# Performance work log

Measured on AMD Instinct MI355X. Metric: run time of the kernel, lower is better.

## Reference

```python
import jax, jax.numpy as jnp
import numpy as np
import math

B, S, D, H = 4, 2048, 1024, 16
HD = D // H  # head_size = 64


def setup_inputs() -> dict:
    key = jax.random.key(0)
    ks = jax.random.split(key, 12)
    s = 1.0 / math.sqrt(D)
    inp = {
        "query_in": jax.random.normal(ks[0], (B, S, D), jnp.float32),
        "key_in": jax.random.normal(ks[1], (B, S, D), jnp.float32),
        "values_in": jax.random.normal(ks[2], (B, S, D), jnp.float32),
        # causal mask, broadcast over batch and heads
        "mask": jnp.tril(jnp.ones((S, S), jnp.int32))[None, None],
        "Wq": jax.random.normal(ks[3], (D, D), jnp.float32) * s,
        "bq": jnp.zeros((D,), jnp.float32),
        "Wk": jax.random.normal(ks[4], (D, D), jnp.float32) * s,
        "bk": jnp.zeros((D,), jnp.float32),
        "Wv": jax.random.normal(ks[5], (D, D), jnp.float32) * s,
        "bv": jnp.zeros((D,), jnp.float32),
        "Wo": jax.random.normal(ks[6], (D, D), jnp.float32) * s,
        "bo": jnp.zeros((D,), jnp.float32),
    }
    return inp


def _heads(x):
    # [B,S,D] -> [B,H,S,HD]
    return x.reshape(B, S, H, HD).transpose(0, 2, 1, 3)


def reference(query_in, key_in, values_in, mask, Wq, bq, Wk, bk, Wv, bv, Wo, bo):
    q = _heads(query_in @ Wq.T + bq)
    k = _heads(key_in @ Wk.T + bk)
    v = _heads(values_in @ Wv.T + bv)
    # scaled dot-product scores [B,H,Sq,Sk]
    att = jnp.einsum("bhqd,bhkd->bhqk", q, k) / math.sqrt(HD)
    att = jnp.where(mask == 0, jnp.float32(-1e9), att)
    # NOTE: original module applies dropout (identity at eval / p=0) directly
    # to scores with NO softmax -- faithfully reproduced here.
    out = jnp.einsum("bhqk,bhkd->bhqd", att, v)
    out = out.transpose(0, 2, 1, 3).reshape(B, S, D)
    return out @ Wo.T + bo
```

## Files before the change

### kernel.cpp

```cpp
#include <hip/hip_runtime.h>
#include <stdint.h>

typedef unsigned short ushort_t;
typedef __bf16 bf16x8 __attribute__((ext_vector_type(8)));
typedef float f32x4 __attribute__((ext_vector_type(4)));
typedef ushort_t us4 __attribute__((ext_vector_type(4)));

#define MFMA16(a, b, c) __builtin_amdgcn_mfma_f32_16x16x32_bf16((a), (b), (c), 0, 0, 0)

constexpr int Bn = 4, Sn = 2048, Dn = 1024, Hn = 16, HDn = 64;
constexpr float SCALE = 0.125f;
constexpr float NEG = -1e9f;

__device__ __forceinline__ float bf2f(ushort_t u) {
  unsigned x = ((unsigned)u) << 16;
  return __builtin_bit_cast(float, x);
}
__device__ __forceinline__ ushort_t f2bf(float f) {
  unsigned x = __builtin_bit_cast(unsigned, f);
  x = x + 0x7FFFu + ((x >> 16) & 1u);
  return (ushort_t)(x >> 16);
}
__device__ __forceinline__ uint4 ld8_f32_bf16(const float* __restrict__ p) {
  float4 a = *(const float4*)p;
  float4 b = *(const float4*)(p + 4);
  union { ushort_t u[8]; uint4 v; } r;
  r.u[0] = f2bf(a.x); r.u[1] = f2bf(a.y); r.u[2] = f2bf(a.z); r.u[3] = f2bf(a.w);
  r.u[4] = f2bf(b.x); r.u[5] = f2bf(b.y); r.u[6] = f2bf(b.z); r.u[7] = f2bf(b.w);
  return r.v;
}
__device__ __forceinline__ void gl2lds16(const void* g, void* l) {
  __builtin_amdgcn_global_load_lds(
      (__attribute__((address_space(1))) void*)g,
      (__attribute__((address_space(3))) void*)l, 16, 0, 0);
}

__global__ __launch_bounds__(256)
void cvt_all(const float* __restrict__ xq, const float* __restrict__ xk,
             const float* __restrict__ xv, const float* __restrict__ wq,
             const float* __restrict__ wk, const float* __restrict__ wv,
             const float* __restrict__ wo, ushort_t* __restrict__ Xd,
             ushort_t* __restrict__ Wd) {
  const int bid = blockIdx.x;
  if (bid < 12288) {
    const int which = bid >> 12;
    const float* s = which == 0 ? xq : which == 1 ? xk : xv;
    size_t i = ((size_t)(bid & 4095) * 256 + threadIdx.x) * 8;
    *(uint4*)(Xd + (size_t)which * 8388608 + i) = ld8_f32_bf16(s + i);
  } else {
    const int wb = bid - 12288, which = wb >> 9;
    const float* s = which == 0 ? wq : which == 1 ? wk : which == 2 ? wv : wo;
    size_t i = ((size_t)(wb & 511) * 256 + threadIdx.x) * 8;
    *(uint4*)(Wd + (size_t)which * 1048576 + i) = ld8_f32_bf16(s + i);
  }
}

__global__ __launch_bounds__(256, 4)
void gemm_qkv(const ushort_t* __restrict__ Xb, const ushort_t* __restrict__ Wb,
              const float* __restrict__ bq, const float* __restrict__ bk,
              const float* __restrict__ bv, ushort_t* __restrict__ Qd,
              ushort_t* __restrict__ Ktd, ushort_t* __restrict__ Vtd) {
  constexpr int K = 1024;
  __shared__ __align__(16) ushort_t As[128 * 64];
  __shared__ __align__(16) ushort_t Bs[128 * 64];

  const int z = blockIdx.z;
  const ushort_t* A  = Xb + (size_t)z * 8388608;
  const ushort_t* Wt = Wb + (size_t)z * 1048576;
  const float* bias = z == 0 ? bq : z == 1 ? bk : bv;
  ushort_t* Cp = z == 0 ? Qd : z == 1 ? Ktd : Vtd;

  const int tid = threadIdx.x;
  const int lane = tid & 63, w = tid >> 6;
  const int quad = lane >> 4, l16 = lane & 15;
  const int wm = w >> 1, wn = w & 1;
  const int row0 = blockIdx.x * 128;
  const int col0 = blockIdx.y * 128;

  const int sr = lane >> 3;
  const int sg = ((lane & 7) ^ (sr & 7)) * 8;
  const ushort_t* Ab = A  + (size_t)(row0 + w * 32 + sr) * K + sg;
  const ushort_t* Bb = Wt + (size_t)(col0 + w * 32 + sr) * K + sg;

  f32x4 acc[4][4] = {};

  for (int k0 = 0; k0 < K; k0 += 64) {
    __syncthreads();
#pragma unroll
    for (int i = 0; i < 4; ++i) {
      gl2lds16(Ab + (size_t)(i * 8) * K + k0, &As[(w * 32 + i * 8) * 64]);
      gl2lds16(Bb + (size_t)(i * 8) * K + k0, &Bs[(w * 32 + i * 8) * 64]);
    }
    __syncthreads();
#pragma unroll
    for (int ks = 0; ks < 2; ++ks) {
      const int kg = ((ks * 4 + quad) ^ (l16 & 7)) * 8;
      bf16x8 af[4], bfr[4];
#pragma unroll
      for (int mt = 0; mt < 4; ++mt)
        af[mt] = *(const bf16x8*)(&As[(wm * 64 + mt * 16 + l16) * 64 + kg]);
#pragma unroll
      for (int nt = 0; nt < 4; ++nt)
        bfr[nt] = *(const bf16x8*)(&Bs[(wn * 64 + nt * 16 + l16) * 64 + kg]);
#pragma unroll
      for (int mt = 0; mt < 4; ++mt)
#pragma unroll
        for (int nt = 0; nt < 4; ++nt)
          acc[mt][nt] = MFMA16(af[mt], bfr[nt], acc[mt][nt]);
    }
  }

#pragma unroll
  for (int mt = 0; mt < 4; ++mt) {
#pragma unroll
    for (int nt = 0; nt < 4; ++nt) {
      const int col = col0 + wn * 64 + nt * 16 + l16;
      const float bv4 = bias[col];
      const int rowb = row0 + wm * 64 + mt * 16 + quad * 4;
      if (z != 0) {
        const int b = rowb >> 11, s = rowb & (Sn - 1);
        const int h = col >> 6, hd = col & 63;
        us4 pk;
#pragma unroll
        for (int r = 0; r < 4; ++r) pk[r] = f2bf(acc[mt][nt][r] + bv4);
        *(us4*)(Cp + ((size_t)((b * Hn + h) * HDn + hd)) * Sn + s) = pk;
      } else {
#pragma unroll
        for (int r = 0; r < 4; ++r) {
          const int row = rowb + r;
          const int b = row >> 11, s = row & (Sn - 1);
          const int h = col >> 6, hd = col & 63;
          Cp[(((size_t)(b * Hn + h) * Sn + s) << 6) + hd] = f2bf(acc[mt][nt][r] + bv4);
        }
      }
    }
  }
}

__global__ __launch_bounds__(256, 4)
void gemm_out(const ushort_t* __restrict__ A, const ushort_t* __restrict__ Wt,
              const float* __restrict__ bias, float* __restrict__ Cp) {
  constexpr int K = 1024;
  __shared__ __align__(16) ushort_t As[128 * 64];
  __shared__ __align__(16) ushort_t Bs[128 * 64];

  const int tid = threadIdx.x;
  const int lane = tid & 63, w = tid >> 6;
  const int quad = lane >> 4, l16 = lane & 15;
  const int wm = w >> 1, wn = w & 1;
  const int row0 = blockIdx.x * 128;
  const int col0 = blockIdx.y * 128;

  const int sr = lane >> 3;
  const int sg = ((lane & 7) ^ (sr & 7)) * 8;
  const ushort_t* Ab = A  + (size_t)(row0 + w * 32 + sr) * K + sg;
  const ushort_t* Bb = Wt + (size_t)(col0 + w * 32 + sr) * K + sg;

  f32x4 acc[4][4] = {};

  for (int k0 = 0; k0 < K; k0 += 64) {
    __syncthreads();
#pragma unroll
    for (int i = 0; i < 4; ++i) {
      gl2lds16(Ab + (size_t)(i * 8) * K + k0, &As[(w * 32 + i * 8) * 64]);
      gl2lds16(Bb + (size_t)(i * 8) * K + k0, &Bs[(w * 32 + i * 8) * 64]);
    }
    __syncthreads();
#pragma unroll
    for (int ks = 0; ks < 2; ++ks) {
      const int kg = ((ks * 4 + quad) ^ (l16 & 7)) * 8;
      bf16x8 af[4], bfr[4];
#pragma unroll
      for (int mt = 0; mt < 4; ++mt)
        af[mt] = *(const bf16x8*)(&As[(wm * 64 + mt * 16 + l16) * 64 + kg]);
#pragma unroll
      for (int nt = 0; nt < 4; ++nt)
        bfr[nt] = *(const bf16x8*)(&Bs[(wn * 64 + nt * 16 + l16) * 64 + kg]);
#pragma unroll
      for (int mt = 0; mt < 4; ++mt)
#pragma unroll
        for (int nt = 0; nt < 4; ++nt)
          acc[mt][nt] = MFMA16(af[mt], bfr[nt], acc[mt][nt]);
    }
  }

#pragma unroll
  for (int mt = 0; mt < 4; ++mt)
#pragma unroll
    for (int nt = 0; nt < 4; ++nt) {
      const int col = col0 + wn * 64 + nt * 16 + l16;
      const float bv = bias[col];
      const int rowb = row0 + wm * 64 + mt * 16 + quad * 4;
#pragma unroll
      for (int r = 0; r < 4; ++r)
        Cp[(size_t)(rowb + r) * 1024 + col] = acc[mt][nt][r] + bv;
    }
}

__global__ __launch_bounds__(256)
void gtile(const ushort_t* __restrict__ Kt, const ushort_t* __restrict__ Vt,
           float* __restrict__ Gd, float* __restrict__ Rs) {
  __shared__ __align__(16) ushort_t Kts[4096];
  __shared__ __align__(16) ushort_t Vts[4096];
  __shared__ float tsum[64];
  const int tid = threadIdx.x, lane = tid & 63, w = tid >> 6;
  const int quad = lane >> 4, l16 = lane & 15;
  const int t = blockIdx.x, bh = blockIdx.y;
  const ushort_t* Ktb = Kt + (size_t)bh * HDn * Sn;
  const ushort_t* Vtb = Vt + (size_t)bh * HDn * Sn;

  const int sr = lane >> 3;
  const int sg = ((lane & 7) ^ (sr & 7)) * 8;

  if (tid < 64) tsum[tid] = 0.f;
#pragma unroll
  for (int c = 0; c < 2; ++c) {
    const int row = w * 16 + c * 8;
    gl2lds16(Ktb + (size_t)(row + sr) * Sn + t * 64 + sg, &Kts[row * 64]);
    gl2lds16(Vtb + (size_t)(row + sr) * Sn + t * 64 + sg, &Vts[row * 64]);
  }
  __syncthreads();

  f32x4 zacc[4] = {};
#pragma unroll
  for (int ks = 0; ks < 2; ++ks) {
    const int kg = ((ks * 4 + quad) ^ (l16 & 7)) * 8;
    bf16x8 ak = *(const bf16x8*)(&Kts[(w * 16 + l16) * 64 + kg]);
#pragma unroll
    for (int nt = 0; nt < 4; ++nt) {
      bf16x8 bv8 = *(const bf16x8*)(&Vts[(nt * 16 + l16) * 64 + kg]);
      zacc[nt] = MFMA16(ak, bv8, zacc[nt]);
    }
  }
  float* gd = Gd + (size_t)(bh * 32 + t) * 4096;
#pragma unroll
  for (int nt = 0; nt < 4; ++nt)
    *(f32x4*)(gd + (nt * 16 + l16) * 64 + w * 16 + quad * 4) = zacc[nt];

  {
    const int n = tid & 63, j = tid >> 6;
    float p = 0.f;
#pragma unroll
    for (int gg2 = 0; gg2 < 2; ++gg2) {
      const int g = 2 * j + gg2;
      union { uint4 v; ushort_t u[8]; } c;
      c.v = *(const uint4*)(&Vts[n * 64 + ((g ^ (n & 7)) << 3)]);
#pragma unroll
      for (int e = 0; e < 8; ++e) p += bf2f(c.u[e]);
    }
    atomicAdd(&tsum[n], p);
  }
  __syncthreads();
  if (tid < 64) Rs[(size_t)(bh * 32 + t) * 64 + tid] = tsum[tid];
}

__global__ __launch_bounds__(256)
void scan_attn(const ushort_t* __restrict__ Q, const ushort_t* __restrict__ Kt,
               const ushort_t* __restrict__ Vt, const float* __restrict__ Gd,
               const float* __restrict__ Rs, ushort_t* __restrict__ O) {
  __shared__ __align__(16) ushort_t Vts[2][4096];
  __shared__ __align__(16) ushort_t Zs[4096];
  __shared__ __align__(16) ushort_t Ks[4096];
  __shared__ __align__(16) ushort_t Ss[64][72];
  __shared__ __align__(16) float sfx[4][64];

  const int tid = threadIdx.x, lane = tid & 63, w = tid >> 6;
  const int quad = lane >> 4, l16 = lane & 15;
  const int bh = blockIdx.x;
  const int g = blockIdx.y;
  const int qt0 = g * 4;
  const int b = bh >> 4, h = bh & 15;
  const ushort_t* Qb  = Q  + (size_t)bh * Sn * HDn;
  const ushort_t* Ktb = Kt + (size_t)bh * HDn * Sn;
  const ushort_t* Vtb = Vt + (size_t)bh * HDn * Sn;
  const float* Gb = Gd + (size_t)bh * 32 * 4096;
  const float* Rb = Rs + (size_t)bh * 32 * 64;

  const int sr = lane >> 3;
  const int sg = ((lane & 7) ^ (sr & 7)) * 8;
  const int q8 = lane & 7, h8 = lane >> 3;

  const int zn = tid >> 2, zd0 = (tid & 3) * 16;
  const float* gthr = Gb + zn * 64 + zd0;

  uint4  kvr[2][2];
  bf16x8 bqr[2][2];
  f32x4  gq[2][4];

  {
    const int q0 = qt0 * 64;
#pragma unroll
    for (int c = 0; c < 2; ++c) {
      const int row = w * 16 + c * 8;
      gl2lds16(Vtb + (size_t)(row + sr) * Sn + q0 + sg, &Vts[0][row * 64]);
      kvr[0][c] = *(const uint4*)(Ktb + (size_t)(w * 16 + c * 8 + h8) * Sn + q0 + q8 * 8);
    }
#pragma unroll
    for (int ks = 0; ks < 2; ++ks)
      bqr[0][ks] = *(const bf16x8*)(Qb + (size_t)(q0 + w * 16 + l16) * HDn + (ks * 4 + quad) * 8);
#pragma unroll
    for (int j = 0; j < 4; ++j)
      gq[0][j] = *(const f32x4*)(gthr + (size_t)qt0 * 4096 + 4 * j);
  }

  if (tid < 64) {
    float acc = 0.f;
    for (int tau = 31; tau >= qt0; --tau) {
      if (tau < qt0 + 4) sfx[tau - qt0][tid] = acc;
      acc += Rb[(size_t)tau * 64 + tid];
    }
  }

  f32x4 Zacc[4] = {};
#pragma unroll 4
  for (int tau = 0; tau < qt0; ++tau) {
#pragma unroll
    for (int j = 0; j < 4; ++j)
      Zacc[j] += *(const f32x4*)(gthr + (size_t)tau * 4096 + 4 * j);
  }

#pragma unroll 4
  for (int i = 0; i < 4; ++i) {
    const int cur = i & 1;
    const int qt = qt0 + i, q0 = qt * 64;

    __syncthreads();

#pragma unroll
    for (int j = 0; j < 4; ++j) {
      const int d = zd0 + 4 * j;
      us4 pk;
#pragma unroll
      for (int r = 0; r < 4; ++r) pk[r] = f2bf(SCALE * Zacc[j][r]);
      *(us4*)(&Zs[zn * 64 + (((d >> 3) ^ (zn & 7)) << 3) + (d & 7)]) = pk;
    }
#pragma unroll
    for (int c = 0; c < 2; ++c) {
      const int hd = w * 16 + c * 8 + h8;
      const int G = hd >> 3;
      const ushort_t* ku = (const ushort_t*)&kvr[cur][c];
#pragma unroll
      for (int j = 0; j < 8; ++j) {
        const int e = (j + q8) & 7;
        const int s = q8 * 8 + e;
        Ks[s * 64 + ((G ^ e) << 3) + (hd & 7)] = ku[e];
      }
    }

    __syncthreads();

    if (i < 3) {
      const int q1 = (qt + 1) * 64, nxt = 1 - cur;
#pragma unroll
      for (int c = 0; c < 2; ++c) {
        const int row = w * 16 + c * 8;
        gl2lds16(Vtb + (size_t)(row + sr) * Sn + q1 + sg, &Vts[nxt][row * 64]);
        kvr[nxt][c] = *(const uint4*)(Ktb + (size_t)(w * 16 + c * 8 + h8) * Sn + q1 + q8 * 8);
      }
#pragma unroll
      for (int ks = 0; ks < 2; ++ks)
        bqr[nxt][ks] = *(const bf16x8*)(Qb + (size_t)(q1 + w * 16 + l16) * HDn + (ks * 4 + quad) * 8);
#pragma unroll
      for (int j = 0; j < 4; ++j)
        gq[nxt][j] = *(const f32x4*)(gthr + (size_t)(qt + 1) * 4096 + 4 * j);
    }

    f32x4 oacc[4] = {};
#pragma unroll
    for (int ks = 0; ks < 2; ++ks) {
      const int kg = ((ks * 4 + quad) ^ (l16 & 7)) * 8;
#pragma unroll
      for (int nt = 0; nt < 4; ++nt) {
        bf16x8 az = *(const bf16x8*)(&Zs[(nt * 16 + l16) * 64 + kg]);
        oacc[nt] = MFMA16(az, bqr[cur][ks], oacc[nt]);
      }
    }
    f32x4 sacc[4] = {};
#pragma unroll
    for (int ks = 0; ks < 2; ++ks) {
      const int kg = ((ks * 4 + quad) ^ (l16 & 7)) * 8;
#pragma unroll
      for (int nt = 0; nt < 4; ++nt) {
        bf16x8 ak = *(const bf16x8*)(&Ks[(nt * 16 + l16) * 64 + kg]);
        sacc[nt] = MFMA16(ak, bqr[cur][ks], sacc[nt]);
      }
    }
    const int qrel = w * 16 + l16;
#pragma unroll
    for (int nt = 0; nt < 4; ++nt) {
      const int kb = nt * 16 + quad * 4;
      us4 pk;
#pragma unroll
      for (int r = 0; r < 4; ++r) {
        float val = (kb + r > qrel) ? NEG : sacc[nt][r] * SCALE;
        pk[r] = f2bf(val);
      }
      *(us4*)(&Ss[qrel][kb]) = pk;
    }
#pragma unroll
    for (int ks = 0; ks < 2; ++ks) {
      bf16x8 bs = *(const bf16x8*)(&Ss[qrel][ks * 32 + quad * 8]);
#pragma unroll
      for (int nt = 0; nt < 4; ++nt) {
        bf16x8 av = *(const bf16x8*)(&Vts[cur][(nt * 16 + l16) * 64 + (((ks * 4 + quad) ^ (l16 & 7)) << 3)]);
        oacc[nt] = MFMA16(av, bs, oacc[nt]);
      }
    }

    const int s = q0 + w * 16 + l16;
#pragma unroll
    for (int nt = 0; nt < 4; ++nt) {
      const int nb = nt * 16 + quad * 4;
      float4 s4 = *(const float4*)(&sfx[i][nb]);
      us4 pk;
      pk[0] = f2bf(oacc[nt][0] + NEG * s4.x);
      pk[1] = f2bf(oacc[nt][1] + NEG * s4.y);
      pk[2] = f2bf(oacc[nt][2] + NEG * s4.z);
      pk[3] = f2bf(oacc[nt][3] + NEG * s4.w);
      *(us4*)(&O[((size_t)(b * Sn + s)) * Dn + h * 64 + nb]) = pk;
    }

#pragma unroll
    for (int j = 0; j < 4; ++j) Zacc[j] += gq[cur][j];
  }
}

extern "C" void kernel_launch(void* const* d_in, const int* in_sizes, int n_in,
                              void* d_out, int out_size, void* d_ws, size_t ws_size,
                              hipStream_t stream) {
  const float* Xq = (const float*)d_in[0];
  const float* Xk = (const float*)d_in[1];
  const float* Xv = (const float*)d_in[2];
  const float* Wq = (const float*)d_in[4];
  const float* bq = (const float*)d_in[5];
  const float* Wk = (const float*)d_in[6];
  const float* bk = (const float*)d_in[7];
  const float* Wv = (const float*)d_in[8];
  const float* bv = (const float*)d_in[9];
  const float* Wo = (const float*)d_in[10];
  const float* bo = (const float*)d_in[11];

  constexpr size_t MiB = 1024 * 1024;
  char* ws = (char*)d_ws;
  ushort_t* Xb  = (ushort_t*)(ws);
  ushort_t* Wb  = (ushort_t*)(ws + 48 * MiB);
  ushort_t* Qb  = (ushort_t*)(ws + 56 * MiB);
  ushort_t* Ktb = (ushort_t*)(ws + 72 * MiB);
  ushort_t* Vtb = (ushort_t*)(ws + 88 * MiB);
  ushort_t* Ob  = (ushort_t*)(ws + 120 * MiB);
  float*    Gd  = (float*)   (ws + 144 * MiB);
  float*    Rsum= (float*)   (ws + 176 * MiB);

  cvt_all<<<14336, 256, 0, stream>>>(Xq, Xk, Xv, Wq, Wk, Wv, Wo, Xb, Wb);
  gemm_qkv<<<dim3(64, 8, 3), 256, 0, stream>>>(Xb, Wb, bq, bk, bv, Qb, Ktb, Vtb);
  gtile<<<dim3(32, 64), 256, 0, stream>>>(Ktb, Vtb, Gd, Rsum);
  scan_attn<<<dim3(64, 8), 256, 0, stream>>>(Qb, Ktb, Vtb, Gd, Rsum, Ob);
  gemm_out<<<dim3(64, 8), 256, 0, stream>>>(Ob, Wb + (size_t)3 * 1048576, bo,
                                            (float*)d_out);
}
```

Measured before the change: 303.5 us.

## Fuse K^T V prefix into scan kernel and V row sums into QKV GEMM

Removes the separate gtile kernel. V tile row sums are now computed in the QKV GEMM epilogue with shuffle reductions, and each scan_attn2 block computes its own K^T V prefix with MFMA over the preceding tiles using double-buffered LDS loads. This drops the fp32 Gd intermediate write and read and one kernel launch. In exchange it repeats prefix work across blocks, so later sequence groups get up to 28 tiles of extra MFMA, giving load imbalance. Row sums are also now taken from fp32 accumulators instead of bf16-rounded V.

New measurement: 290.7 us. -4.2%, faster.

```diff
diff --git a/kernel.cpp b/kernel.cpp
--- a/kernel.cpp
+++ b/kernel.cpp
@@ -59,7 +59,8 @@
 void gemm_qkv(const ushort_t* __restrict__ Xb, const ushort_t* __restrict__ Wb,
               const float* __restrict__ bq, const float* __restrict__ bk,
               const float* __restrict__ bv, ushort_t* __restrict__ Qd,
-              ushort_t* __restrict__ Ktd, ushort_t* __restrict__ Vtd) {
+              ushort_t* __restrict__ Ktd, ushort_t* __restrict__ Vtd,
+              float* __restrict__ Rs) {
   constexpr int K = 1024;
   __shared__ __align__(16) ushort_t As[128 * 64];
   __shared__ __align__(16) ushort_t Bs[128 * 64];
@@ -135,6 +136,27 @@
       }
     }
   }
+
+  if (z == 2) {
+    const int b = row0 >> 11;
+    const int t = ((row0 & (Sn - 1)) >> 6) + wm;
+#pragma unroll
+    for (int nt = 0; nt < 4; ++nt) {
+      const int col = col0 + wn * 64 + nt * 16 + l16;
+      const float bv4 = bias[col];
+      float p = 0.f;
+#pragma unroll
+      for (int mt = 0; mt < 4; ++mt)
+#pragma unroll
+        for (int r = 0; r < 4; ++r) p += acc[mt][nt][r] + bv4;
+      p += __shfl_xor(p, 16);
+      p += __shfl_xor(p, 32);
+      if (quad == 0) {
+        const int h = col >> 6, n = col & 63;
+        Rs[((size_t)(b * Hn + h) * 32 + t) * 64 + n] = p;
+      }
+    }
+  }
 }
 
 __global__ __launch_bounds__(256, 4)
@@ -198,66 +220,10 @@
 }
 
 __global__ __launch_bounds__(256)
-void gtile(const ushort_t* __restrict__ Kt, const ushort_t* __restrict__ Vt,
-           float* __restrict__ Gd, float* __restrict__ Rs) {
-  __shared__ __align__(16) ushort_t Kts[4096];
-  __shared__ __align__(16) ushort_t Vts[4096];
-  __shared__ float tsum[64];
-  const int tid = threadIdx.x, lane = tid & 63, w = tid >> 6;
-  const int quad = lane >> 4, l16 = lane & 15;
-  const int t = blockIdx.x, bh = blockIdx.y;
-  const ushort_t* Ktb = Kt + (size_t)bh * HDn * Sn;
-  const ushort_t* Vtb = Vt + (size_t)bh * HDn * Sn;
-
-  const int sr = lane >> 3;
-  const int sg = ((lane & 7) ^ (sr & 7)) * 8;
-
-  if (tid < 64) tsum[tid] = 0.f;
-#pragma unroll
-  for (int c = 0; c < 2; ++c) {
-    const int row = w * 16 + c * 8;
-    gl2lds16(Ktb + (size_t)(row + sr) * Sn + t * 64 + sg, &Kts[row * 64]);
-    gl2lds16(Vtb + (size_t)(row + sr) * Sn + t * 64 + sg, &Vts[row * 64]);
-  }
-  __syncthreads();
-
-  f32x4 zacc[4] = {};
-#pragma unroll
-  for (int ks = 0; ks < 2; ++ks) {
-    const int kg = ((ks * 4 + quad) ^ (l16 & 7)) * 8;
-    bf16x8 ak = *(const bf16x8*)(&Kts[(w * 16 + l16) * 64 + kg]);
-#pragma unroll
-    for (int nt = 0; nt < 4; ++nt) {
-      bf16x8 bv8 = *(const bf16x8*)(&Vts[(nt * 16 + l16) * 64 + kg]);
-      zacc[nt] = MFMA16(ak, bv8, zacc[nt]);
-    }
-  }
-  float* gd = Gd + (size_t)(bh * 32 + t) * 4096;
-#pragma unroll
-  for (int nt = 0; nt < 4; ++nt)
-    *(f32x4*)(gd + (nt * 16 + l16) * 64 + w * 16 + quad * 4) = zacc[nt];
-
-  {
-    const int n = tid & 63, j = tid >> 6;
-    float p = 0.f;
-#pragma unroll
-    for (int gg2 = 0; gg2 < 2; ++gg2) {
-      const int g = 2 * j + gg2;
-      union { uint4 v; ushort_t u[8]; } c;
-      c.v = *(const uint4*)(&Vts[n * 64 + ((g ^ (n & 7)) << 3)]);
-#pragma unroll
-      for (int e = 0; e < 8; ++e) p += bf2f(c.u[e]);
-    }
-    atomicAdd(&tsum[n], p);
-  }
-  __syncthreads();
-  if (tid < 64) Rs[(size_t)(bh * 32 + t) * 64 + tid] = tsum[tid];
-}
-
-__global__ __launch_bounds__(256)
-void scan_attn(const ushort_t* __restrict__ Q, const ushort_t* __restrict__ Kt,
-               const ushort_t* __restrict__ Vt, const float* __restrict__ Gd,
-               const float* __restrict__ Rs, ushort_t* __restrict__ O) {
+void scan_attn2(const ushort_t* __restrict__ Q, const ushort_t* __restrict__ Kt,
+                const ushort_t* __restrict__ Vt, const float* __restrict__ Rs,
+                ushort_t* __restrict__ O) {
+  __shared__ __align__(16) ushort_t Kp[2][4096];
   __shared__ __align__(16) ushort_t Vts[2][4096];
   __shared__ __align__(16) ushort_t Zs[4096];
   __shared__ __align__(16) ushort_t Ks[4096];
@@ -273,20 +239,47 @@
   const ushort_t* Qb  = Q  + (size_t)bh * Sn * HDn;
   const ushort_t* Ktb = Kt + (size_t)bh * HDn * Sn;
   const ushort_t* Vtb = Vt + (size_t)bh * HDn * Sn;
-  const float* Gb = Gd + (size_t)bh * 32 * 4096;
   const float* Rb = Rs + (size_t)bh * 32 * 64;
 
   const int sr = lane >> 3;
   const int sg = ((lane & 7) ^ (sr & 7)) * 8;
   const int q8 = lane & 7, h8 = lane >> 3;
 
-  const int zn = tid >> 2, zd0 = (tid & 3) * 16;
-  const float* gthr = Gb + zn * 64 + zd0;
+  f32x4 pzacc[4] = {};
+  if (qt0 > 0) {
+#pragma unroll
+    for (int c = 0; c < 2; ++c) {
+      const int row = w * 16 + c * 8;
+      gl2lds16(Ktb + (size_t)(row + sr) * Sn + sg, &Kp[0][row * 64]);
+      gl2lds16(Vtb + (size_t)(row + sr) * Sn + sg, &Vts[0][row * 64]);
+    }
+    for (int tau = 0; tau < qt0; ++tau) {
+      const int pc = tau & 1;
+      __syncthreads();
+      if (tau + 1 < qt0) {
+#pragma unroll
+        for (int c = 0; c < 2; ++c) {
+          const int row = w * 16 + c * 8;
+          gl2lds16(Ktb + (size_t)(row + sr) * Sn + (tau + 1) * 64 + sg, &Kp[1 - pc][row * 64]);
+          gl2lds16(Vtb + (size_t)(row + sr) * Sn + (tau + 1) * 64 + sg, &Vts[1 - pc][row * 64]);
+        }
+      }
+#pragma unroll
+      for (int ks = 0; ks < 2; ++ks) {
+        const int kg = ((ks * 4 + quad) ^ (l16 & 7)) * 8;
+        bf16x8 ak = *(const bf16x8*)(&Kp[pc][(w * 16 + l16) * 64 + kg]);
+#pragma unroll
+        for (int nt = 0; nt < 4; ++nt) {
+          bf16x8 bv8 = *(const bf16x8*)(&Vts[pc][(nt * 16 + l16) * 64 + kg]);
+          pzacc[nt] = MFMA16(ak, bv8, pzacc[nt]);
+        }
+      }
+    }
+    __syncthreads();
+  }
 
   uint4  kvr[2][2];
   bf16x8 bqr[2][2];
-  f32x4  gq[2][4];
-
   {
     const int q0 = qt0 * 64;
 #pragma unroll
@@ -298,9 +291,6 @@
 #pragma unroll
     for (int ks = 0; ks < 2; ++ks)
       bqr[0][ks] = *(const bf16x8*)(Qb + (size_t)(q0 + w * 16 + l16) * HDn + (ks * 4 + quad) * 8);
-#pragma unroll
-    for (int j = 0; j < 4; ++j)
-      gq[0][j] = *(const f32x4*)(gthr + (size_t)qt0 * 4096 + 4 * j);
   }
 
   if (tid < 64) {
@@ -311,14 +301,6 @@
     }
   }
 
-  f32x4 Zacc[4] = {};
-#pragma unroll 4
-  for (int tau = 0; tau < qt0; ++tau) {
-#pragma unroll
-    for (int j = 0; j < 4; ++j)
-      Zacc[j] += *(const f32x4*)(gthr + (size_t)tau * 4096 + 4 * j);
-  }
-
 #pragma unroll 4
   for (int i = 0; i < 4; ++i) {
     const int cur = i & 1;
@@ -327,12 +309,13 @@
     __syncthreads();
 
 #pragma unroll
-    for (int j = 0; j < 4; ++j) {
-      const int d = zd0 + 4 * j;
+    for (int nt = 0; nt < 4; ++nt) {
+      const int n = nt * 16 + l16;
+      const int d0 = w * 16 + quad * 4;
       us4 pk;
 #pragma unroll
-      for (int r = 0; r < 4; ++r) pk[r] = f2bf(SCALE * Zacc[j][r]);
-      *(us4*)(&Zs[zn * 64 + (((d >> 3) ^ (zn & 7)) << 3) + (d & 7)]) = pk;
+      for (int r = 0; r < 4; ++r) pk[r] = f2bf(SCALE * pzacc[nt][r]);
+      *(us4*)(&Zs[n * 64 + (((d0 >> 3) ^ (n & 7)) << 3) + (d0 & 7)]) = pk;
     }
 #pragma unroll
     for (int c = 0; c < 2; ++c) {
@@ -346,6 +329,11 @@
         Ks[s * 64 + ((G ^ e) << 3) + (hd & 7)] = ku[e];
       }
     }
+#pragma unroll
+    for (int c = 0; c < 2; ++c) {
+      const int hd = w * 16 + c * 8 + h8;
+      *(uint4*)(&Kp[0][hd * 64 + ((q8 ^ (hd & 7)) << 3)]) = kvr[cur][c];
+    }
 
     __syncthreads();
 
@@ -360,9 +348,6 @@
 #pragma unroll
       for (int ks = 0; ks < 2; ++ks)
         bqr[nxt][ks] = *(const bf16x8*)(Qb + (size_t)(q1 + w * 16 + l16) * HDn + (ks * 4 + quad) * 8);
-#pragma unroll
-      for (int j = 0; j < 4; ++j)
-        gq[nxt][j] = *(const f32x4*)(gthr + (size_t)(qt + 1) * 4096 + 4 * j);
     }
 
     f32x4 oacc[4] = {};
@@ -420,8 +405,18 @@
       *(us4*)(&O[((size_t)(b * Sn + s)) * Dn + h * 64 + nb]) = pk;
     }
 
-#pragma unroll
-    for (int j = 0; j < 4; ++j) Zacc[j] += gq[cur][j];
+    if (i < 3) {
+#pragma unroll
+      for (int ks = 0; ks < 2; ++ks) {
+        const int kg = ((ks * 4 + quad) ^ (l16 & 7)) * 8;
+        bf16x8 ak = *(const bf16x8*)(&Kp[0][(w * 16 + l16) * 64 + kg]);
+#pragma unroll
+        for (int nt = 0; nt < 4; ++nt) {
+          bf16x8 bv8 = *(const bf16x8*)(&Vts[cur][(nt * 16 + l16) * 64 + kg]);
+          pzacc[nt] = MFMA16(ak, bv8, pzacc[nt]);
+        }
+      }
+    }
   }
 }
 
@@ -448,13 +443,12 @@
   ushort_t* Ktb = (ushort_t*)(ws + 72 * MiB);
   ushort_t* Vtb = (ushort_t*)(ws + 88 * MiB);
   ushort_t* Ob  = (ushort_t*)(ws + 120 * MiB);
-  float*    Gd  = (float*)   (ws + 144 * MiB);
   float*    Rsum= (float*)   (ws + 176 * MiB);
 
   cvt_all<<<14336, 256, 0, stream>>>(Xq, Xk, Xv, Wq, Wk, Wv, Wo, Xb, Wb);
-  gemm_qkv<<<dim3(64, 8, 3), 256, 0, stream>>>(Xb, Wb, bq, bk, bv, Qb, Ktb, Vtb);
-  gtile<<<dim3(32, 64), 256, 0, stream>>>(Ktb, Vtb, Gd, Rsum);
-  scan_attn<<<dim3(64, 8), 256, 0, stream>>>(Qb, Ktb, Vtb, Gd, Rsum, Ob);
+  gemm_qkv<<<dim3(64, 8, 3), 256, 0, stream>>>(Xb, Wb, bq, bk, bv, Qb, Ktb,
+                                               Vtb, Rsum);
+  scan_attn2<<<dim3(64, 8), 256, 0, stream>>>(Qb, Ktb, Vtb, Rsum, Ob);
   gemm_out<<<dim3(64, 8), 256, 0, stream>>>(Ob, Wb + (size_t)3 * 1048576, bo,
                                             (float*)d_out);
 }
```
